# Kernel optimization log

Measured on AMD Instinct MI355X. Metric: run time of the kernel, lower is better.

Reference implementation:

```python
import jax, jax.numpy as jnp
import numpy as np

BETA = 0.25


def setup_inputs() -> dict:
    key = jax.random.key(0)
    k1, k2 = jax.random.split(key)
    inputs = jax.random.normal(k1, (16, 64, 64, 256), dtype=jnp.float32)
    # codebook, shape (embedding_dim=256, num_embeddings=1024), uniform init like tf
    embeddings = jax.random.uniform(k2, (256, 1024), dtype=jnp.float32)
    return {"inputs": inputs, "embeddings": embeddings}


def reference(inputs, embeddings):
    D = embeddings.shape[0]
    flat = inputs.reshape(-1, D)  # [N, D]
    distances = (
        jnp.sum(flat * flat, axis=1, keepdims=True)
        - 2.0 * (flat @ embeddings)
        + jnp.sum(embeddings * embeddings, axis=0, keepdims=True)
    )
    encoding_indices = jnp.argmin(distances, axis=1)  # == argmax(-d)
    # one_hot @ embeddings.T is just a row gather from the codebook
    quantized = jnp.take(embeddings.T, encoding_indices, axis=0).reshape(inputs.shape)
    commitment_loss = BETA * jnp.mean(
        (jax.lax.stop_gradient(quantized) - inputs) ** 2
    )
    # straight-through estimator
    quantized = inputs + jax.lax.stop_gradient(quantized - inputs)
    return quantized, commitment_loss, encoding_indices
```

## Files before the change

### kernel.cpp

```cpp
#include <hip/hip_runtime.h>
#include <float.h>

typedef _Float16 half8 __attribute__((ext_vector_type(8)));
typedef float    f32x4 __attribute__((ext_vector_type(4)));

#define N_ROWS   65536
#define DIM      256
#define KCODES   1024
#define VQ_BETA  0.25
#define MARGIN   2.5f
#define HCAP     512

__global__ void transpose_e(const float* __restrict__ E, float* __restrict__ Et) {
    __shared__ float t[32][33];
    const int kt = blockIdx.x * 32;
    const int dt = blockIdx.y * 32;
    const int lx = threadIdx.x & 31;
    const int ly = threadIdx.x >> 5;
#pragma unroll
    for (int i = 0; i < 4; ++i) {
        int d = dt + ly + i * 8;
        t[ly + i * 8][lx] = E[(size_t)d * KCODES + kt + lx];
    }
    __syncthreads();
#pragma unroll
    for (int i = 0; i < 4; ++i) {
        int k = kt + ly + i * 8;
        Et[(size_t)k * DIM + dt + lx] = t[lx][ly + i * 8];
    }
}

__global__ void enorm_kernel(const float* __restrict__ E, float* __restrict__ enorm) {
    const int k = blockIdx.x * 256 + threadIdx.x;
    float s = 0.f;
#pragma unroll 4
    for (int d = 0; d < DIM; ++d) {
        float v = E[(size_t)d * KCODES + k];
        s = fmaf(v, v, s);
    }
    enorm[k] = s;
}

__global__ void efrag_kernel(const float* __restrict__ Et, _Float16* __restrict__ Efb) {
    const int fid = blockIdx.x * 256 + threadIdx.x;
    const int lhi   = fid & 3;
    const int llo   = (fid >> 2) & 15;
    const int nt    = (fid >> 6) & 3;
    const int w     = (fid >> 8) & 3;
    const int slice = fid >> 10;
    const int chunk = slice >> 3, ks = slice & 7;
    const int code  = chunk * 256 + w * 64 + nt * 16 + llo;
    const float* src = Et + (size_t)code * DIM + ks * 32 + lhi * 8;
    half8 h;
#pragma unroll
    for (int j = 0; j < 8; ++j) h[j] = (_Float16)src[j];
    *reinterpret_cast<half8*>(Efb + (size_t)fid * 8) = h;
}

__device__ __forceinline__ void load_bf(const _Float16* __restrict__ eb,
                                        half8 (&bf)[4]) {
    bf[0] = *reinterpret_cast<const half8*>(eb);
    bf[1] = *reinterpret_cast<const half8*>(eb + 512);
    bf[2] = *reinterpret_cast<const half8*>(eb + 1024);
    bf[3] = *reinterpret_cast<const half8*>(eb + 1536);
}
__device__ __forceinline__ void load_af(const char* AhB, int ks, int llo, int lhi,
                                        int aswz, half8 (&af)[4]) {
#pragma unroll
    for (int mt = 0; mt < 4; ++mt) {
        const int addr = ((mt * 16 + llo) * 512 + (ks * 4 + lhi) * 16) ^ aswz;
        af[mt] = *reinterpret_cast<const half8*>(AhB + addr);
    }
}
__device__ __forceinline__ void mfma16(const half8 (&af)[4], const half8 (&bf)[4],
                                       f32x4 (&acc)[4][4]) {
#pragma unroll
    for (int mt = 0; mt < 4; ++mt)
#pragma unroll
        for (int nt = 0; nt < 4; ++nt)
            acc[mt][nt] = __builtin_amdgcn_mfma_f32_16x16x32_f16(
                af[mt], bf[nt], acc[mt][nt], 0, 0, 0);
}
__device__ __forceinline__ void mfma_chunk(
        const _Float16* __restrict__ ebase, const char* AhB,
        int llo, int lhi, int aswz, f32x4 (&acc)[4][4]) {
    half8 bfa[4], bfb[4], af[4];
    load_bf(ebase, bfa);
#pragma unroll
    for (int ks2 = 0; ks2 < 4; ++ks2) {
        const int ksA = ks2 * 2, ksB = ks2 * 2 + 1;
        load_bf(ebase + (size_t)ksB * 8192, bfb);
        load_af(AhB, ksA, llo, lhi, aswz, af);
        mfma16(af, bfa, acc);
        if (ksB < 7) load_bf(ebase + (size_t)(ksB + 1) * 8192, bfa);
        load_af(AhB, ksB, llo, lhi, aswz, af);
        mfma16(af, bfb, acc);
    }
}

__global__ __launch_bounds__(256, 2) void vq_mfma(
        const float* __restrict__ X, const _Float16* __restrict__ Efb,
        const float* __restrict__ enorm, const float* __restrict__ Et,
        float* __restrict__ outidx, float* __restrict__ outq,
        float* __restrict__ partials)
{
    __shared__ _Float16 Ah[64 * 256];
    __shared__ float    x2s[64];
    __shared__ float    bminw[4][64];
    __shared__ float    cutoff_s[64];
    __shared__ unsigned minb[64], mini[64];
    __shared__ int      hits[HCAP];
    __shared__ float    dstore[HCAP];
    __shared__ unsigned hitcnt;
    __shared__ int      ovf;

    const int tid = threadIdx.x;
    const int rowbase = blockIdx.x * 64;

    if (tid == 0) { hitcnt = 0; ovf = 0; }
    if (tid < 64) { minb[tid] = 0xFFFFFFFFu; mini[tid] = 0xFFFFFFFFu; }

    {
        const int row = tid >> 2;
        float x2p = 0.f;
#pragma unroll
        for (int i = 0; i < 8; ++i) {
            const int g = (tid & 3) + 4 * i;
            const float* src = X + (size_t)(rowbase + row) * DIM + g * 8;
            float4 a = *reinterpret_cast<const float4*>(src);
            float4 b = *reinterpret_cast<const float4*>(src + 4);
            x2p = fmaf(a.x, a.x, x2p); x2p = fmaf(a.y, a.y, x2p);
            x2p = fmaf(a.z, a.z, x2p); x2p = fmaf(a.w, a.w, x2p);
            x2p = fmaf(b.x, b.x, x2p); x2p = fmaf(b.y, b.y, x2p);
            x2p = fmaf(b.z, b.z, x2p); x2p = fmaf(b.w, b.w, x2p);
            half8 h;
            h[0] = (_Float16)a.x; h[1] = (_Float16)a.y;
            h[2] = (_Float16)a.z; h[3] = (_Float16)a.w;
            h[4] = (_Float16)b.x; h[5] = (_Float16)b.y;
            h[6] = (_Float16)b.z; h[7] = (_Float16)b.w;
            const int addr = (row * 512 + g * 16) ^ ((row & 7) << 4);
            *reinterpret_cast<half8*>(reinterpret_cast<char*>(Ah) + addr) = h;
        }
        x2p += __shfl_xor(x2p, 1, 64);
        x2p += __shfl_xor(x2p, 2, 64);
        if ((tid & 3) == 0) x2s[row] = x2p;
    }
    __syncthreads();

    const int w    = tid >> 6;
    const int lane = tid & 63;
    const int lhi  = lane >> 4, llo = lane & 15;
    const int aswz = (llo & 7) << 4;
    const int lane_off8 = (llo * 4 + lhi) * 8;
    const char* AhB = reinterpret_cast<const char*>(Ah);

    float minv[16];
#pragma unroll
    for (int sl = 0; sl < 16; ++sl) minv[sl] = FLT_MAX;

    for (int chunk = 0; chunk < 4; ++chunk) {
        f32x4 acc[4][4];
#pragma unroll
        for (int mt = 0; mt < 4; ++mt)
#pragma unroll
            for (int nt = 0; nt < 4; ++nt) acc[mt][nt] = (f32x4){0.f, 0.f, 0.f, 0.f};

        const _Float16* ebase = Efb + (size_t)chunk * 65536 + w * 2048 + lane_off8;
        mfma_chunk(ebase, AhB, llo, lhi, aswz, acc);

#pragma unroll
        for (int nt = 0; nt < 4; ++nt) {
            const float e2 = enorm[chunk * 256 + w * 64 + nt * 16 + llo];
#pragma unroll
            for (int mt = 0; mt < 4; ++mt)
#pragma unroll
                for (int q = 0; q < 4; ++q)
                    minv[mt * 4 + q] = fminf(minv[mt * 4 + q],
                                             fmaf(-2.0f, acc[mt][nt][q], e2));
        }
    }
#pragma unroll
    for (int m = 1; m < 16; m <<= 1)
#pragma unroll
        for (int sl = 0; sl < 16; ++sl)
            minv[sl] = fminf(minv[sl], __shfl_xor(minv[sl], m, 64));
    if (llo == 0) {
#pragma unroll
        for (int mt = 0; mt < 4; ++mt)
#pragma unroll
            for (int q = 0; q < 4; ++q)
                bminw[w][mt * 16 + lhi * 4 + q] = minv[mt * 4 + q];
    }
    __syncthreads();
    if (tid < 64)
        cutoff_s[tid] = fminf(fminf(bminw[0][tid], bminw[1][tid]),
                              fminf(bminw[2][tid], bminw[3][tid])) + MARGIN;
    __syncthreads();

    float cut[16];
#pragma unroll
    for (int mt = 0; mt < 4; ++mt)
#pragma unroll
        for (int q = 0; q < 4; ++q)
            cut[mt * 4 + q] = cutoff_s[mt * 16 + lhi * 4 + q];

    for (int chunk = 0; chunk < 4; ++chunk) {
        f32x4 acc[4][4];
#pragma unroll
        for (int mt = 0; mt < 4; ++mt)
#pragma unroll
            for (int nt = 0; nt < 4; ++nt) acc[mt][nt] = (f32x4){0.f, 0.f, 0.f, 0.f};

        const _Float16* ebase = Efb + (size_t)chunk * 65536 + w * 2048 + lane_off8;
        mfma_chunk(ebase, AhB, llo, lhi, aswz, acc);

#pragma unroll
        for (int nt = 0; nt < 4; ++nt) {
            const int code = chunk * 256 + w * 64 + nt * 16 + llo;
            const float e2 = enorm[code];
#pragma unroll
            for (int mt = 0; mt < 4; ++mt)
#pragma unroll
                for (int q = 0; q < 4; ++q) {
                    const float ds = fmaf(-2.0f, acc[mt][nt][q], e2);
                    if (ds < cut[mt * 4 + q]) {
                        const unsigned p = atomicAdd(&hitcnt, 1u);
                        if (p < HCAP)
                            hits[p] = ((mt * 16 + lhi * 4 + q) << 10) | code;
                        else
                            ovf = 1;
                    }
                }
        }
    }
    __syncthreads();

    const int nh = (int)(hitcnt < HCAP ? hitcnt : (unsigned)HCAP);

    if (!ovf) {
        for (int hi = tid; hi < nh; hi += 256) {
            const int pk = hits[hi];
            const int rl = pk >> 10, code = pk & 1023;
            const float* xr = X  + (size_t)(rowbase + rl) * DIM;
            const float* er = Et + (size_t)code * DIM;
            float p = 0.f, x2 = 0.f;
#pragma unroll
            for (int j = 0; j < 64; ++j) {
                float4 xv = *reinterpret_cast<const float4*>(xr + j * 4);
                float4 ev = *reinterpret_cast<const float4*>(er + j * 4);
                x2 = fmaf(xv.x, xv.x, x2); x2 = fmaf(xv.y, xv.y, x2);
                x2 = fmaf(xv.z, xv.z, x2); x2 = fmaf(xv.w, xv.w, x2);
                p  = fmaf(xv.x, ev.x, p);  p  = fmaf(xv.y, ev.y, p);
                p  = fmaf(xv.z, ev.z, p);  p  = fmaf(xv.w, ev.w, p);
            }
            const float dd = (x2 - 2.0f * p) + enorm[code];
            dstore[hi] = dd;
            atomicMin(&minb[rl], __float_as_uint(dd));
        }
        __syncthreads();
        for (int hi = tid; hi < nh; hi += 256) {
            const int pk = hits[hi];
            const int rl = pk >> 10;
            if (__float_as_uint(dstore[hi]) == minb[rl])
                atomicMin(&mini[rl], (unsigned)(pk & 1023));
        }
    } else {
        const int rl = tid >> 2, part = tid & 3;
        const float* xr = X + (size_t)(rowbase + rl) * DIM;
        float bd = FLT_MAX; int bk = 0;
        for (int c = part; c < KCODES; c += 4) {
            const float* er = Et + (size_t)c * DIM;
            float p = 0.f;
#pragma unroll 4
            for (int d = 0; d < DIM; d += 4) {
                float4 xv = *reinterpret_cast<const float4*>(xr + d);
                float4 ev = *reinterpret_cast<const float4*>(er + d);
                p = fmaf(xv.x, ev.x, p); p = fmaf(xv.y, ev.y, p);
                p = fmaf(xv.z, ev.z, p); p = fmaf(xv.w, ev.w, p);
            }
            const float dd = (x2s[rl] - 2.0f * p) + enorm[c];
            if (dd < bd) { bd = dd; bk = c; }
        }
        atomicMin(&minb[rl], __float_as_uint(bd));
        __syncthreads();
        if (__float_as_uint(bd) == minb[rl])
            atomicMin(&mini[rl], (unsigned)bk);
    }
    __syncthreads();

    float* red = dstore;
    {
        const int row  = tid >> 2;
        const int part = tid & 3;
        const int cw   = (int)mini[row];
        const float* xrow = X  + (size_t)(rowbase + row) * DIM;
        const float* ew   = Et + (size_t)cw * DIM;
        float* oq = outq + (size_t)(rowbase + row) * DIM;
        if (part == 0) outidx[rowbase + row] = (float)cw;

        float lsum = 0.f;
#pragma unroll
        for (int j = 0; j < 16; ++j) {
            const int d0 = j * 16 + part * 4;
            float4 q = *reinterpret_cast<const float4*>(ew + d0);
            float4 x = *reinterpret_cast<const float4*>(xrow + d0);
            float4 o;
            o.x = x.x + (q.x - x.x);
            o.y = x.y + (q.y - x.y);
            o.z = x.z + (q.z - x.z);
            o.w = x.w + (q.w - x.w);
            *reinterpret_cast<float4*>(oq + d0) = o;
            float dx;
            dx = q.x - x.x; lsum = fmaf(dx, dx, lsum);
            dx = q.y - x.y; lsum = fmaf(dx, dx, lsum);
            dx = q.z - x.z; lsum = fmaf(dx, dx, lsum);
            dx = q.w - x.w; lsum = fmaf(dx, dx, lsum);
        }
        red[tid] = lsum;
    }
    __syncthreads();
    for (int s = 128; s > 0; s >>= 1) {
        if (tid < s) red[tid] += red[tid + s];
        __syncthreads();
    }
    if (tid == 0) partials[blockIdx.x] = red[0];
}

__global__ void loss_final(const float* __restrict__ partials, float* __restrict__ out) {
    __shared__ double sd[256];
    const int tid = threadIdx.x;
    double s = 0.0;
    for (int i = tid; i < 1024; i += 256) s += (double)partials[i];
    sd[tid] = s;
    __syncthreads();
    for (int k = 128; k > 0; k >>= 1) {
        if (tid < k) sd[tid] += sd[tid + k];
        __syncthreads();
    }
    if (tid == 0) out[0] = (float)(VQ_BETA * sd[0] / (double)((size_t)N_ROWS * DIM));
}

extern "C" void kernel_launch(void* const* d_in, const int* in_sizes, int n_in,
                              void* d_out, int out_size, void* d_ws, size_t ws_size,
                              hipStream_t stream) {
    const float* X = (const float*)d_in[0];
    const float* E = (const float*)d_in[1];

    float* outq    = (float*)d_out;
    float* outloss = outq + (size_t)N_ROWS * DIM;
    float* outidx  = outloss + 1;

    float*    Et       = (float*)d_ws;
    _Float16* Efb      = (_Float16*)(Et + 262144);
    float*    enormw   = (float*)(Efb + 262144);
    float*    partials = enormw + KCODES;

    transpose_e <<<dim3(32, 8), 256, 0, stream>>>(E, Et);
    enorm_kernel<<<4,           256, 0, stream>>>(E, enormw);
    efrag_kernel<<<128,         256, 0, stream>>>(Et, Efb);
    vq_mfma     <<<N_ROWS / 64, 256, 0, stream>>>(X, Efb, enormw, Et,
                                                  outidx, outq, partials);
    loss_final  <<<1,           256, 0, stream>>>(partials, outloss);
}
```

Before: 180.2 us.

## Fuse two-pass MFMA distance scan into single pass with running cutoff and per-row fallback

Drops the second full MFMA pass over the codebook. The kernel now computes distances once, updating a running per-row minimum and cutoff after each chunk and collecting candidates against it. The overflow fallback now does an exact full-codebook search only for the rows that overflowed, instead of the whole block. Margin and hit capacity are also retuned. This roughly halves the tensor-core work, at the cost of extra barriers per chunk and more candidates from early chunks while the running cutoff is still loose.

```diff
diff --git a/kernel.cpp b/kernel.cpp
--- a/kernel.cpp
+++ b/kernel.cpp
@@ -8,8 +8,8 @@
 #define DIM      256
 #define KCODES   1024
 #define VQ_BETA  0.25
-#define MARGIN   2.5f
-#define HCAP     512
+#define MARGIN   1.5f
+#define HCAP     640
 
 __global__ void transpose_e(const float* __restrict__ E, float* __restrict__ Et) {
     __shared__ float t[32][33];
@@ -105,34 +105,32 @@
         float* __restrict__ partials)
 {
     __shared__ _Float16 Ah[64 * 256];
-    __shared__ float    x2s[64];
     __shared__ float    bminw[4][64];
     __shared__ float    cutoff_s[64];
+    __shared__ float    rmin_s[64];
     __shared__ unsigned minb[64], mini[64];
+    __shared__ int      rowbad[64];
     __shared__ int      hits[HCAP];
     __shared__ float    dstore[HCAP];
     __shared__ unsigned hitcnt;
-    __shared__ int      ovf;
 
     const int tid = threadIdx.x;
     const int rowbase = blockIdx.x * 64;
 
-    if (tid == 0) { hitcnt = 0; ovf = 0; }
-    if (tid < 64) { minb[tid] = 0xFFFFFFFFu; mini[tid] = 0xFFFFFFFFu; }
+    if (tid == 0) hitcnt = 0;
+    if (tid < 64) {
+        minb[tid] = 0xFFFFFFFFu; mini[tid] = 0xFFFFFFFFu;
+        rmin_s[tid] = FLT_MAX;   rowbad[tid] = 0;
+    }
 
     {
         const int row = tid >> 2;
-        float x2p = 0.f;
 #pragma unroll
         for (int i = 0; i < 8; ++i) {
             const int g = (tid & 3) + 4 * i;
             const float* src = X + (size_t)(rowbase + row) * DIM + g * 8;
             float4 a = *reinterpret_cast<const float4*>(src);
             float4 b = *reinterpret_cast<const float4*>(src + 4);
-            x2p = fmaf(a.x, a.x, x2p); x2p = fmaf(a.y, a.y, x2p);
-            x2p = fmaf(a.z, a.z, x2p); x2p = fmaf(a.w, a.w, x2p);
-            x2p = fmaf(b.x, b.x, x2p); x2p = fmaf(b.y, b.y, x2p);
-            x2p = fmaf(b.z, b.z, x2p); x2p = fmaf(b.w, b.w, x2p);
             half8 h;
             h[0] = (_Float16)a.x; h[1] = (_Float16)a.y;
             h[2] = (_Float16)a.z; h[3] = (_Float16)a.w;
@@ -141,9 +139,6 @@
             const int addr = (row * 512 + g * 16) ^ ((row & 7) << 4);
             *reinterpret_cast<half8*>(reinterpret_cast<char*>(Ah) + addr) = h;
         }
-        x2p += __shfl_xor(x2p, 1, 64);
-        x2p += __shfl_xor(x2p, 2, 64);
-        if ((tid & 3) == 0) x2s[row] = x2p;
     }
     __syncthreads();
 
@@ -154,10 +149,6 @@
     const int lane_off8 = (llo * 4 + lhi) * 8;
     const char* AhB = reinterpret_cast<const char*>(Ah);
 
-    float minv[16];
-#pragma unroll
-    for (int sl = 0; sl < 16; ++sl) minv[sl] = FLT_MAX;
-
     for (int chunk = 0; chunk < 4; ++chunk) {
         f32x4 acc[4][4];
 #pragma unroll
@@ -168,125 +159,133 @@
         const _Float16* ebase = Efb + (size_t)chunk * 65536 + w * 2048 + lane_off8;
         mfma_chunk(ebase, AhB, llo, lhi, aswz, acc);
 
-#pragma unroll
-        for (int nt = 0; nt < 4; ++nt) {
-            const float e2 = enorm[chunk * 256 + w * 64 + nt * 16 + llo];
+        float e2v[4];
+#pragma unroll
+        for (int nt = 0; nt < 4; ++nt)
+            e2v[nt] = enorm[chunk * 256 + w * 64 + nt * 16 + llo];
+
+        float mloc[16];
+#pragma unroll
+        for (int mt = 0; mt < 4; ++mt)
+#pragma unroll
+            for (int q = 0; q < 4; ++q) {
+                float m = FLT_MAX;
+#pragma unroll
+                for (int nt = 0; nt < 4; ++nt) {
+                    const float ds = fmaf(-2.0f, acc[mt][nt][q], e2v[nt]);
+                    acc[mt][nt][q] = ds;
+                    m = fminf(m, ds);
+                }
+                mloc[mt * 4 + q] = m;
+            }
+#pragma unroll
+        for (int m = 1; m < 16; m <<= 1)
+#pragma unroll
+            for (int sl = 0; sl < 16; ++sl)
+                mloc[sl] = fminf(mloc[sl], __shfl_xor(mloc[sl], m, 64));
+        if (llo == 0) {
 #pragma unroll
             for (int mt = 0; mt < 4; ++mt)
 #pragma unroll
                 for (int q = 0; q < 4; ++q)
-                    minv[mt * 4 + q] = fminf(minv[mt * 4 + q],
-                                             fmaf(-2.0f, acc[mt][nt][q], e2));
-        }
-    }
-#pragma unroll
-    for (int m = 1; m < 16; m <<= 1)
-#pragma unroll
-        for (int sl = 0; sl < 16; ++sl)
-            minv[sl] = fminf(minv[sl], __shfl_xor(minv[sl], m, 64));
-    if (llo == 0) {
+                    bminw[w][mt * 16 + lhi * 4 + q] = mloc[mt * 4 + q];
+        }
+        __syncthreads();
+        if (tid < 64) {
+            float r = fminf(fminf(bminw[0][tid], bminw[1][tid]),
+                            fminf(bminw[2][tid], bminw[3][tid]));
+            r = fminf(rmin_s[tid], r);
+            rmin_s[tid]   = r;
+            cutoff_s[tid] = r + MARGIN;
+        }
+        __syncthreads();
+
 #pragma unroll
         for (int mt = 0; mt < 4; ++mt)
 #pragma unroll
-            for (int q = 0; q < 4; ++q)
-                bminw[w][mt * 16 + lhi * 4 + q] = minv[mt * 4 + q];
-    }
-    __syncthreads();
-    if (tid < 64)
-        cutoff_s[tid] = fminf(fminf(bminw[0][tid], bminw[1][tid]),
-                              fminf(bminw[2][tid], bminw[3][tid])) + MARGIN;
-    __syncthreads();
-
-    float cut[16];
-#pragma unroll
-    for (int mt = 0; mt < 4; ++mt)
-#pragma unroll
-        for (int q = 0; q < 4; ++q)
-            cut[mt * 4 + q] = cutoff_s[mt * 16 + lhi * 4 + q];
-
-    for (int chunk = 0; chunk < 4; ++chunk) {
-        f32x4 acc[4][4];
-#pragma unroll
-        for (int mt = 0; mt < 4; ++mt)
-#pragma unroll
-            for (int nt = 0; nt < 4; ++nt) acc[mt][nt] = (f32x4){0.f, 0.f, 0.f, 0.f};
-
-        const _Float16* ebase = Efb + (size_t)chunk * 65536 + w * 2048 + lane_off8;
-        mfma_chunk(ebase, AhB, llo, lhi, aswz, acc);
-
-#pragma unroll
-        for (int nt = 0; nt < 4; ++nt) {
-            const int code = chunk * 256 + w * 64 + nt * 16 + llo;
-            const float e2 = enorm[code];
-#pragma unroll
-            for (int mt = 0; mt < 4; ++mt)
-#pragma unroll
-                for (int q = 0; q < 4; ++q) {
-                    const float ds = fmaf(-2.0f, acc[mt][nt][q], e2);
-                    if (ds < cut[mt * 4 + q]) {
+            for (int q = 0; q < 4; ++q) {
+                const int row = mt * 16 + lhi * 4 + q;
+                const float cut = cutoff_s[row];
+#pragma unroll
+                for (int nt = 0; nt < 4; ++nt) {
+                    if (acc[mt][nt][q] < cut) {
                         const unsigned p = atomicAdd(&hitcnt, 1u);
                         if (p < HCAP)
-                            hits[p] = ((mt * 16 + lhi * 4 + q) << 10) | code;
+                            hits[p] = (row << 10) |
+                                      (chunk * 256 + w * 64 + nt * 16 + llo);
                         else
-                            ovf = 1;
+                            rowbad[row] = 1;
                     }
                 }
-        }
+            }
     }
     __syncthreads();
 
     const int nh = (int)(hitcnt < HCAP ? hitcnt : (unsigned)HCAP);
 
-    if (!ovf) {
-        for (int hi = tid; hi < nh; hi += 256) {
-            const int pk = hits[hi];
-            const int rl = pk >> 10, code = pk & 1023;
-            const float* xr = X  + (size_t)(rowbase + rl) * DIM;
-            const float* er = Et + (size_t)code * DIM;
-            float p = 0.f, x2 = 0.f;
-#pragma unroll
-            for (int j = 0; j < 64; ++j) {
-                float4 xv = *reinterpret_cast<const float4*>(xr + j * 4);
-                float4 ev = *reinterpret_cast<const float4*>(er + j * 4);
-                x2 = fmaf(xv.x, xv.x, x2); x2 = fmaf(xv.y, xv.y, x2);
-                x2 = fmaf(xv.z, xv.z, x2); x2 = fmaf(xv.w, xv.w, x2);
-                p  = fmaf(xv.x, ev.x, p);  p  = fmaf(xv.y, ev.y, p);
-                p  = fmaf(xv.z, ev.z, p);  p  = fmaf(xv.w, ev.w, p);
-            }
-            const float dd = (x2 - 2.0f * p) + enorm[code];
-            dstore[hi] = dd;
-            atomicMin(&minb[rl], __float_as_uint(dd));
-        }
-        __syncthreads();
-        for (int hi = tid; hi < nh; hi += 256) {
-            const int pk = hits[hi];
-            const int rl = pk >> 10;
-            if (__float_as_uint(dstore[hi]) == minb[rl])
-                atomicMin(&mini[rl], (unsigned)(pk & 1023));
-        }
-    } else {
-        const int rl = tid >> 2, part = tid & 3;
-        const float* xr = X + (size_t)(rowbase + rl) * DIM;
-        float bd = FLT_MAX; int bk = 0;
-        for (int c = part; c < KCODES; c += 4) {
-            const float* er = Et + (size_t)c * DIM;
-            float p = 0.f;
-#pragma unroll 4
-            for (int d = 0; d < DIM; d += 4) {
-                float4 xv = *reinterpret_cast<const float4*>(xr + d);
-                float4 ev = *reinterpret_cast<const float4*>(er + d);
-                p = fmaf(xv.x, ev.x, p); p = fmaf(xv.y, ev.y, p);
-                p = fmaf(xv.z, ev.z, p); p = fmaf(xv.w, ev.w, p);
-            }
-            const float dd = (x2s[rl] - 2.0f * p) + enorm[c];
-            if (dd < bd) { bd = dd; bk = c; }
-        }
-        atomicMin(&minb[rl], __float_as_uint(bd));
-        __syncthreads();
-        if (__float_as_uint(bd) == minb[rl])
-            atomicMin(&mini[rl], (unsigned)bk);
-    }
-    __syncthreads();
+    for (int hi = tid; hi < nh; hi += 256) {
+        const int pk = hits[hi];
+        const int rl = pk >> 10, code = pk & 1023;
+        const float* xr = X  + (size_t)(rowbase + rl) * DIM;
+        const float* er = Et + (size_t)code * DIM;
+        float p = 0.f, x2 = 0.f;
+#pragma unroll
+        for (int j = 0; j < 64; ++j) {
+            float4 xv = *reinterpret_cast<const float4*>(xr + j * 4);
+            float4 ev = *reinterpret_cast<const float4*>(er + j * 4);
+            x2 = fmaf(xv.x, xv.x, x2); x2 = fmaf(xv.y, xv.y, x2);
+            x2 = fmaf(xv.z, xv.z, x2); x2 = fmaf(xv.w, xv.w, x2);
+            p  = fmaf(xv.x, ev.x, p);  p  = fmaf(xv.y, ev.y, p);
+            p  = fmaf(xv.z, ev.z, p);  p  = fmaf(xv.w, ev.w, p);
+        }
+        const float dd = (x2 - 2.0f * p) + enorm[code];
+        dstore[hi] = dd;
+        atomicMin(&minb[rl], __float_as_uint(dd));
+    }
+    __syncthreads();
+    for (int hi = tid; hi < nh; hi += 256) {
+        const int pk = hits[hi];
+        const int rl = pk >> 10;
+        if (__float_as_uint(dstore[hi]) == minb[rl])
+            atomicMin(&mini[rl], (unsigned)(pk & 1023));
+    }
+    __syncthreads();
+
+    float* xs = dstore;
+    for (int r = 0; r < 64; ++r) {
+        if (!rowbad[r]) continue;
+        xs[tid] = X[(size_t)(rowbase + r) * DIM + tid];
+        __syncthreads();
+        float x2 = 0.f;
+        for (int d = 0; d < DIM; ++d) x2 = fmaf(xs[d], xs[d], x2);
+        float a0 = 0.f, a1 = 0.f, a2 = 0.f, a3 = 0.f;
+        const float* e0 = Et + (size_t)(tid      ) * DIM;
+        const float* e1 = Et + (size_t)(tid + 256) * DIM;
+        const float* e2p = Et + (size_t)(tid + 512) * DIM;
+        const float* e3 = Et + (size_t)(tid + 768) * DIM;
+        for (int d = 0; d < DIM; ++d) {
+            const float xv = xs[d];
+            a0 = fmaf(xv, e0[d], a0);
+            a1 = fmaf(xv, e1[d], a1);
+            a2 = fmaf(xv, e2p[d], a2);
+            a3 = fmaf(xv, e3[d], a3);
+        }
+        const float d0 = (x2 - 2.0f * a0) + enorm[tid];
+        const float d1 = (x2 - 2.0f * a1) + enorm[tid + 256];
+        const float d2 = (x2 - 2.0f * a2) + enorm[tid + 512];
+        const float d3 = (x2 - 2.0f * a3) + enorm[tid + 768];
+        atomicMin(&minb[r], __float_as_uint(d0));
+        atomicMin(&minb[r], __float_as_uint(d1));
+        atomicMin(&minb[r], __float_as_uint(d2));
+        atomicMin(&minb[r], __float_as_uint(d3));
+        __syncthreads();
+        const unsigned mb = minb[r];
+        if (__float_as_uint(d0) == mb) atomicMin(&mini[r], (unsigned)tid);
+        if (__float_as_uint(d1) == mb) atomicMin(&mini[r], (unsigned)(tid + 256));
+        if (__float_as_uint(d2) == mb) atomicMin(&mini[r], (unsigned)(tid + 512));
+        if (__float_as_uint(d3) == mb) atomicMin(&mini[r], (unsigned)(tid + 768));
+        __syncthreads();
+    }
 
     float* red = dstore;
     {
@@ -316,6 +315,7 @@
             dx = q.z - x.z; lsum = fmaf(dx, dx, lsum);
             dx = q.w - x.w; lsum = fmaf(dx, dx, lsum);
         }
+        __syncthreads();
         red[tid] = lsum;
     }
     __syncthreads();
```

Result: faster. 172.7 us (-4.2%).
